# Performance work log

Hardware: AMD Instinct MI355X
Metric: run time of the kernel (lower is better)

## Reference

```python
import jax, jax.numpy as jnp
import numpy as np

N = 50000
E = 800000
EPS = 1e-5


def graph_conv(x, src, dst, ew, W_rel, b_rel, W_root):
    # PyG GraphConv (aggr='add'): lin_rel(sum_j e_ij * x_j) + lin_root(x_i)
    msg = x[src] * ew[:, None]                      # [E, F_in]
    agg = jax.ops.segment_sum(msg, dst, num_segments=N)  # [N, F_in]
    return agg @ W_rel.T + b_rel + x @ W_root.T


def batchnorm_relu(h, gamma, beta):
    mu = jnp.mean(h, axis=0)
    var = jnp.mean(jnp.square(h - mu), axis=0)
    hn = (h - mu) * jax.lax.rsqrt(var + EPS)
    return jax.nn.relu(hn * gamma + beta)


def setup_inputs() -> dict:
    key = jax.random.key(0)
    ks = jax.random.split(key, 16)
    d_in, h, d_out = 128, 256, 64

    def lin(k, fo, fi):
        return jax.random.normal(k, (fo, fi), jnp.float32) * (1.0 / np.sqrt(fi))

    return {
        "x": jax.random.normal(ks[0], (N, d_in), jnp.float32),
        "edge_index": jax.random.randint(ks[1], (2, E), 0, N, jnp.int32),
        "edge_weight": jax.random.uniform(ks[2], (E,), jnp.float32),
        "Wr0": lin(ks[3], h, d_in), "br0": jnp.zeros((h,), jnp.float32), "Wt0": lin(ks[4], h, d_in),
        "g0": jnp.ones((h,), jnp.float32), "be0": jnp.zeros((h,), jnp.float32),
        "Wr1": lin(ks[5], h, h), "br1": jnp.zeros((h,), jnp.float32), "Wt1": lin(ks[6], h, h),
        "g1": jnp.ones((h,), jnp.float32), "be1": jnp.zeros((h,), jnp.float32),
        "Wr2": lin(ks[7], d_out, h), "br2": jnp.zeros((d_out,), jnp.float32), "Wt2": lin(ks[8], d_out, h),
    }


def reference(x, edge_index, edge_weight, Wr0, br0, Wt0, g0, be0,
              Wr1, br1, Wt1, g1, be1, Wr2, br2, Wt2):
    src, dst = edge_index[0], edge_index[1]
    h = graph_conv(x, src, dst, edge_weight, Wr0, br0, Wt0)
    h = batchnorm_relu(h, g0, be0)
    h = graph_conv(h, src, dst, edge_weight, Wr1, br1, Wt1)
    h = batchnorm_relu(h, g1, be1)
    return graph_conv(h, src, dst, edge_weight, Wr2, br2, Wt2)
```

## Files before the change

kernel.cpp:

```cpp
#include <hip/hip_runtime.h>
#include <cstddef>
#include <cstdint>

#define SCAN_B 512

using bf16x8 = __attribute__((ext_vector_type(8))) short;
using f32x4  = __attribute__((ext_vector_type(4))) float;

__device__ __forceinline__ unsigned short f2bf(float f) {
    unsigned int u = __builtin_bit_cast(unsigned int, f);
    return (unsigned short)((u + 0x7FFFu + ((u >> 16) & 1u)) >> 16);
}
__device__ __forceinline__ float bf2f(unsigned short b) {
    unsigned int u = ((unsigned int)b) << 16;
    return __builtin_bit_cast(float, u);
}
__device__ __forceinline__ float i2f(int i) { return __builtin_bit_cast(float, i); }
__device__ __forceinline__ float u2f(unsigned int u) { return __builtin_bit_cast(float, u); }
__device__ __forceinline__ void gload_lds16(const void* g, void* l) {
    __builtin_amdgcn_global_load_lds((const __attribute__((address_space(1))) void*)g,
                                     (__attribute__((address_space(3))) void*)l, 16, 0, 0);
}

__global__ void hist_conv_k(const int* __restrict__ dst, int* __restrict__ counts,
                            int* __restrict__ rank, int E, int histBlocks,
                            const float* __restrict__ x, const float* __restrict__ Wr0,
                            const float* __restrict__ Wt0, const float* __restrict__ Wr1,
                            const float* __restrict__ Wt1, const float* __restrict__ Wr2,
                            const float* __restrict__ Wt2, unsigned short* __restrict__ x_bf,
                            unsigned short* __restrict__ Wr0b, unsigned short* __restrict__ Wt0b,
                            unsigned short* __restrict__ Wr1b, unsigned short* __restrict__ Wt1b,
                            unsigned short* __restrict__ Wr2b, unsigned short* __restrict__ Wt2b,
                            int n4x) {
    if ((int)blockIdx.x < histBlocks) {
        int e = blockIdx.x * 256 + threadIdx.x;
        if (e < E) rank[e] = atomicAdd(&counts[dst[e]], 1);
        return;
    }
    int j = (blockIdx.x - histBlocks) * 256 + threadIdx.x;
    const float* s;
    unsigned short* d;
    if (j < n4x) { s = x; d = x_bf; }
    else {
        j -= n4x;
        if (j < 8192) { s = Wr0; d = Wr0b; }
        else { j -= 8192;
        if (j < 8192) { s = Wt0; d = Wt0b; }
        else { j -= 8192;
        if (j < 16384) { s = Wr1; d = Wr1b; }
        else { j -= 16384;
        if (j < 16384) { s = Wt1; d = Wt1b; }
        else { j -= 16384;
        if (j < 4096) { s = Wr2; d = Wr2b; }
        else { j -= 4096;
        if (j >= 4096) return;
        s = Wt2; d = Wt2b; } } } } }
    }
    float4 v = reinterpret_cast<const float4*>(s)[j];
    ushort4 o;
    o.x = f2bf(v.x); o.y = f2bf(v.y); o.z = f2bf(v.z); o.w = f2bf(v.w);
    reinterpret_cast<ushort4*>(d)[j] = o;
}

__global__ void scan1_k(const int* __restrict__ counts, int* __restrict__ partial,
                        int* __restrict__ blocksum, int Nn) {
    __shared__ int sh[SCAN_B];
    int i = blockIdx.x * SCAN_B + threadIdx.x;
    int v = (i < Nn) ? counts[i] : 0;
    sh[threadIdx.x] = v;
    __syncthreads();
    for (int off = 1; off < SCAN_B; off <<= 1) {
        int t = (threadIdx.x >= (unsigned)off) ? sh[threadIdx.x - off] : 0;
        __syncthreads();
        sh[threadIdx.x] += t;
        __syncthreads();
    }
    if (i < Nn) partial[i] = sh[threadIdx.x];
    if (threadIdx.x == SCAN_B - 1) blocksum[blockIdx.x] = sh[threadIdx.x];
}

__global__ void scan3b_k(const int* __restrict__ partial, const int* __restrict__ blocksum,
                         int* __restrict__ offsets, int Nn) {
    __shared__ int add_s;
    int bx = blockIdx.x;
    if (threadIdx.x < 64) {
        int s = 0;
        for (int j = threadIdx.x; j < bx; j += 64) s += blocksum[j];
        #pragma unroll
        for (int off = 32; off > 0; off >>= 1) s += __shfl_down(s, off, 64);
        if (threadIdx.x == 0) add_s = s;
    }
    __syncthreads();
    int i = bx * SCAN_B + threadIdx.x;
    if (i >= Nn) return;
    offsets[i + 1] = partial[i] + add_s;
    if (i == 0) offsets[0] = 0;
}

__global__ void fill2_k(const int* __restrict__ src, const int* __restrict__ dst,
                        const float* __restrict__ ew, const int* __restrict__ offsets,
                        const int* __restrict__ rank, int2* __restrict__ e_sw, int E) {
    int e = blockIdx.x * blockDim.x + threadIdx.x;
    if (e >= E) return;
    int pos = offsets[dst[e]] + rank[e];
    e_sw[pos] = make_int2(src[e], __builtin_bit_cast(int, ew[e]));
}

__global__ void gather128_k(const unsigned short* __restrict__ x, const int* __restrict__ offsets,
                            const int2* __restrict__ e_sw, unsigned short* __restrict__ agg, int Nn) {
    int wid = __builtin_amdgcn_readfirstlane((blockIdx.x * blockDim.x + threadIdx.x) >> 6);
    int lane = threadIdx.x & 63;
    if (wid >= Nn) return;
    int p = offsets[wid], end = offsets[wid + 1];
    const char* xb = (const char*)x;
    const unsigned loff = lane * 4u;
    float a0 = 0.f, a1 = 0.f;
    for (; p + 8 <= end; p += 8) {
        int2 ee[8];
        #pragma unroll
        for (int i = 0; i < 8; ++i) ee[i] = e_sw[p + i];
        unsigned vv[8];
        #pragma unroll
        for (int i = 0; i < 8; ++i)
            vv[i] = *reinterpret_cast<const unsigned*>(xb + ((unsigned)ee[i].x * 256u + loff));
        #pragma unroll
        for (int i = 0; i < 8; ++i) {
            float w = i2f(ee[i].y);
            a0 += w * u2f(vv[i] << 16); a1 += w * u2f(vv[i] & 0xFFFF0000u);
        }
    }
    for (; p < end; ++p) {
        int2 e0 = e_sw[p];
        unsigned v0 = *reinterpret_cast<const unsigned*>(xb + ((unsigned)e0.x * 256u + loff));
        float w = i2f(e0.y);
        a0 += w * u2f(v0 << 16); a1 += w * u2f(v0 & 0xFFFF0000u);
    }
    unsigned o = (unsigned)f2bf(a0) | ((unsigned)f2bf(a1) << 16);
    *reinterpret_cast<unsigned*>(agg + (size_t)wid * 128 + lane * 2) = o;
}

__global__ void gather_bn_k(const unsigned short* __restrict__ h_raw,
                            const float* __restrict__ sums, const float* __restrict__ sumsq,
                            const float* __restrict__ g, const float* __restrict__ be,
                            const int* __restrict__ offsets, const int2* __restrict__ e_sw,
                            unsigned short* __restrict__ agg, unsigned short* __restrict__ hN,
                            float invN, int Nn, int gBlocks) {
    const int lane = threadIdx.x & 63;
    if ((int)blockIdx.x >= gBlocks) {
        int total4 = Nn * 64;
        int stride = (gridDim.x - gBlocks) * 256;
        for (int t = (blockIdx.x - gBlocks) * 256 + threadIdx.x; t < total4; t += stride) {
            int f0 = (t & 63) * 4;
            float4 sm = *reinterpret_cast<const float4*>(sums + f0);
            float4 sq = *reinterpret_cast<const float4*>(sumsq + f0);
            float4 gg = *reinterpret_cast<const float4*>(g + f0);
            float4 bb = *reinterpret_cast<const float4*>(be + f0);
            float smv[4] = {sm.x, sm.y, sm.z, sm.w};
            float sqv[4] = {sq.x, sq.y, sq.z, sq.w};
            float ggv[4] = {gg.x, gg.y, gg.z, gg.w};
            float bbv[4] = {bb.x, bb.y, bb.z, bb.w};
            ushort4 v = reinterpret_cast<const ushort4*>(h_raw)[t];
            unsigned short vv[4] = {v.x, v.y, v.z, v.w};
            ushort4 o;
            unsigned short* op = &o.x;
            #pragma unroll
            for (int c = 0; c < 4; ++c) {
                float mu = smv[c] * invN;
                float var = sqv[c] * invN - mu * mu;
                float sc = ggv[c] * rsqrtf(var + 1e-5f);
                float sh = bbv[c] - mu * sc;
                op[c] = f2bf(fmaxf(bf2f(vv[c]) * sc + sh, 0.f));
            }
            reinterpret_cast<ushort4*>(hN)[t] = o;
        }
        return;
    }
    int wid = __builtin_amdgcn_readfirstlane((blockIdx.x * blockDim.x + threadIdx.x) >> 6);
    if (wid >= Nn) return;
    int f0 = lane * 4;
    float4 sm = *reinterpret_cast<const float4*>(sums + f0);
    float4 sq = *reinterpret_cast<const float4*>(sumsq + f0);
    float4 gg = *reinterpret_cast<const float4*>(g + f0);
    float4 bb = *reinterpret_cast<const float4*>(be + f0);
    float sc0, sc1, sc2, sc3, sh0, sh1, sh2, sh3;
    {
        float mu, var;
        mu = sm.x * invN; var = sq.x * invN - mu * mu; sc0 = gg.x * rsqrtf(var + 1e-5f); sh0 = bb.x - mu * sc0;
        mu = sm.y * invN; var = sq.y * invN - mu * mu; sc1 = gg.y * rsqrtf(var + 1e-5f); sh1 = bb.y - mu * sc1;
        mu = sm.z * invN; var = sq.z * invN - mu * mu; sc2 = gg.z * rsqrtf(var + 1e-5f); sh2 = bb.z - mu * sc2;
        mu = sm.w * invN; var = sq.w * invN - mu * mu; sc3 = gg.w * rsqrtf(var + 1e-5f); sh3 = bb.w - mu * sc3;
    }
    int p = offsets[wid], end = offsets[wid + 1];
    const char* xb = (const char*)h_raw;
    const unsigned loff = lane * 8u;
    float a0 = 0.f, a1 = 0.f, a2 = 0.f, a3 = 0.f;
    for (; p + 8 <= end; p += 8) {
        int2 ee[8];
        #pragma unroll
        for (int i = 0; i < 8; ++i) ee[i] = e_sw[p + i];
        uint2 vv[8];
        #pragma unroll
        for (int i = 0; i < 8; ++i)
            vv[i] = *reinterpret_cast<const uint2*>(xb + ((unsigned)ee[i].x * 512u + loff));
        #pragma unroll
        for (int i = 0; i < 8; ++i) {
            float w = i2f(ee[i].y);
            a0 += w * fmaxf(u2f(vv[i].x << 16) * sc0 + sh0, 0.f);
            a1 += w * fmaxf(u2f(vv[i].x & 0xFFFF0000u) * sc1 + sh1, 0.f);
            a2 += w * fmaxf(u2f(vv[i].y << 16) * sc2 + sh2, 0.f);
            a3 += w * fmaxf(u2f(vv[i].y & 0xFFFF0000u) * sc3 + sh3, 0.f);
        }
    }
    for (; p < end; ++p) {
        int2 e0 = e_sw[p];
        uint2 v0 = *reinterpret_cast<const uint2*>(xb + ((unsigned)e0.x * 512u + loff));
        float w = i2f(e0.y);
        a0 += w * fmaxf(u2f(v0.x << 16) * sc0 + sh0, 0.f);
        a1 += w * fmaxf(u2f(v0.x & 0xFFFF0000u) * sc1 + sh1, 0.f);
        a2 += w * fmaxf(u2f(v0.y << 16) * sc2 + sh2, 0.f);
        a3 += w * fmaxf(u2f(v0.y & 0xFFFF0000u) * sc3 + sh3, 0.f);
    }
    uint2 o;
    o.x = (unsigned)f2bf(a0) | ((unsigned)f2bf(a1) << 16);
    o.y = (unsigned)f2bf(a2) | ((unsigned)f2bf(a3) << 16);
    *reinterpret_cast<uint2*>(agg + (size_t)wid * 256 + lane * 4) = o;
}

__global__ void gather_out_k(const unsigned short* __restrict__ t, const float* __restrict__ root,
                             const int* __restrict__ offsets, const int2* __restrict__ e_sw,
                             float* __restrict__ out, int Nn) {
    int gt = blockIdx.x * blockDim.x + threadIdx.x;
    int node = gt >> 4;
    int li = gt & 15;
    if (node >= Nn) return;
    int p = offsets[node], end = offsets[node + 1];
    const char* tb = (const char*)t;
    const unsigned loff = li * 8u;
    float a0 = 0.f, a1 = 0.f, a2 = 0.f, a3 = 0.f;
    for (; p + 8 <= end; p += 8) {
        int2 ee[8];
        #pragma unroll
        for (int i = 0; i < 8; ++i) ee[i] = e_sw[p + i];
        uint2 vv[8];
        #pragma unroll
        for (int i = 0; i < 8; ++i)
            vv[i] = *reinterpret_cast<const uint2*>(tb + ((unsigned)ee[i].x * 128u + loff));
        #pragma unroll
        for (int i = 0; i < 8; ++i) {
            float w = i2f(ee[i].y);
            a0 += w * u2f(vv[i].x << 16); a1 += w * u2f(vv[i].x & 0xFFFF0000u);
            a2 += w * u2f(vv[i].y << 16); a3 += w * u2f(vv[i].y & 0xFFFF0000u);
        }
    }
    for (; p < end; ++p) {
        int2 e0 = e_sw[p];
        uint2 v0 = *reinterpret_cast<const uint2*>(tb + ((unsigned)e0.x * 128u + loff));
        float w = i2f(e0.y);
        a0 += w * u2f(v0.x << 16); a1 += w * u2f(v0.x & 0xFFFF0000u);
        a2 += w * u2f(v0.y << 16); a3 += w * u2f(v0.y & 0xFFFF0000u);
    }
    float4 r = *reinterpret_cast<const float4*>(root + (size_t)node * 64 + li * 4);
    float4 o = make_float4(r.x + a0, r.y + a1, r.z + a2, r.w + a3);
    *reinterpret_cast<float4*>(out + (size_t)node * 64 + li * 4) = o;
}

template<int K, int O, int MODE>
__global__ __launch_bounds__(512, 4) void gemm_mfma_k(
        const unsigned short* __restrict__ A, const unsigned short* __restrict__ Wa,
        const unsigned short* __restrict__ X, const unsigned short* __restrict__ Wb,
        const float* __restrict__ bias, unsigned short* __restrict__ out_bf,
        float* __restrict__ out_f, float* __restrict__ sums, float* __restrict__ sumsq,
        int Nn) {
    constexpr int BM = 128, BN = 128;
    constexpr int MI = 4;
    constexpr int OJ = 2;
    constexpr int KSTEPS = K / 32;
    constexpr int NT = (MODE == 0 ? 2 : 1) * KSTEPS;
    __shared__ unsigned short As[2][BM * 32];
    __shared__ unsigned short Bs[2][BN * 32];
    const int tid = threadIdx.x;
    const int w = tid >> 6, l = tid & 63;
    const int wr = w >> 2, wc = w & 3;
    const int lrow = l & 15, kgrp = l >> 4;
    int bx = blockIdx.x;
    bx = (bx & 7) * (gridDim.x >> 3) + (bx >> 3);
    const int m0 = bx * BM;
    const int n0 = blockIdx.y * BN;
    const int srow = tid >> 2, sslot = tid & 3;
    const int gslot = sslot ^ ((srow >> 1) & 3);

    auto stage = [&](int buf, int t) {
        int ph = t / KSTEPS;
        int k0 = (t % KSTEPS) * 32;
        const unsigned short* Ap = (MODE == 0 && ph) ? X : A;
        const unsigned short* Wp = (MODE == 0 && ph) ? Wb : Wa;
        gload_lds16(Ap + (size_t)(m0 + srow) * K + k0 + (gslot << 3), &As[buf][w * 512]);
        gload_lds16(Wp + (size_t)(n0 + srow) * K + k0 + (gslot << 3), &Bs[buf][w * 512]);
    };

    f32x4 acc[MI][OJ];
    #pragma unroll
    for (int i = 0; i < MI; ++i)
        #pragma unroll
        for (int j = 0; j < OJ; ++j) {
            f32x4 z = {0.f, 0.f, 0.f, 0.f};
            acc[i][j] = z;
        }

    stage(0, 0);
    #pragma unroll
    for (int t = 0; t < NT; ++t) {
        const int cur = t & 1;
        asm volatile("s_waitcnt vmcnt(0)" ::: "memory");
        __builtin_amdgcn_sched_barrier(0);
        __builtin_amdgcn_s_barrier();
        __builtin_amdgcn_sched_barrier(0);
        if (t + 1 < NT) stage(cur ^ 1, t + 1);
        bf16x8 a[MI], b[OJ];
        #pragma unroll
        for (int mi = 0; mi < MI; ++mi) {
            int row = wr * 64 + mi * 16 + lrow;
            int slot = kgrp ^ ((row >> 1) & 3);
            a[mi] = *reinterpret_cast<const bf16x8*>(&As[cur][row * 32 + slot * 8]);
        }
        #pragma unroll
        for (int oj = 0; oj < OJ; ++oj) {
            int row = wc * 32 + oj * 16 + lrow;
            int slot = kgrp ^ ((row >> 1) & 3);
            b[oj] = *reinterpret_cast<const bf16x8*>(&Bs[cur][row * 32 + slot * 8]);
        }
        #pragma unroll
        for (int mi = 0; mi < MI; ++mi)
            #pragma unroll
            for (int oj = 0; oj < OJ; ++oj)
                acc[mi][oj] = __builtin_amdgcn_mfma_f32_16x16x32_bf16(
                    a[mi], b[oj], acc[mi][oj], 0, 0, 0);
    }

    if constexpr (MODE == 0) {
        #pragma unroll
        for (int oj = 0; oj < OJ; ++oj) {
            int col = n0 + wc * 32 + oj * 16 + lrow;
            float bcol = bias[col];
            float s = 0.f, q = 0.f;
            #pragma unroll
            for (int mi = 0; mi < MI; ++mi) {
                #pragma unroll
                for (int r = 0; r < 4; ++r) {
                    int row = m0 + wr * 64 + mi * 16 + kgrp * 4 + r;
                    float v = acc[mi][oj][r] + bcol;
                    if (row < Nn) {
                        out_bf[(size_t)row * O + col] = f2bf(v);
                        s += v; q += v * v;
                    }
                }
            }
            s += __shfl_xor(s, 16, 64); q += __shfl_xor(q, 16, 64);
            s += __shfl_xor(s, 32, 64); q += __shfl_xor(q, 32, 64);
            if (kgrp == 0) {
                atomicAdd(&sums[col], s);
                atomicAdd(&sumsq[col], q);
            }
        }
    } else {
        #pragma unroll
        for (int oj = 0; oj < OJ; ++oj) {
            int col = n0 + wc * 32 + oj * 16 + lrow;
            #pragma unroll
            for (int mi = 0; mi < MI; ++mi) {
                #pragma unroll
                for (int r = 0; r < 4; ++r) {
                    int row = m0 + wr * 64 + mi * 16 + kgrp * 4 + r;
                    if (row < Nn) {
                        if (col < 64)
                            out_bf[(size_t)row * 64 + col] = f2bf(acc[mi][oj][r]);
                        else
                            out_f[(size_t)row * 64 + (col - 64)] = acc[mi][oj][r] + bias[col - 64];
                    }
                }
            }
        }
    }
}

__global__ void bn_relu_bf_k(const unsigned short* __restrict__ h, const float* __restrict__ sums,
                             const float* __restrict__ sumsq, const float* __restrict__ g,
                             const float* __restrict__ be, unsigned short* __restrict__ hb,
                             float invN, int total4) {
    int t = blockIdx.x * blockDim.x + threadIdx.x;
    if (t >= total4) return;
    int f0 = (t & 63) * 4;
    float4 sm = *reinterpret_cast<const float4*>(sums + f0);
    float4 sq = *reinterpret_cast<const float4*>(sumsq + f0);
    float4 gg = *reinterpret_cast<const float4*>(g + f0);
    float4 bb = *reinterpret_cast<const float4*>(be + f0);
    float smv[4] = {sm.x, sm.y, sm.z, sm.w};
    float sqv[4] = {sq.x, sq.y, sq.z, sq.w};
    float ggv[4] = {gg.x, gg.y, gg.z, gg.w};
    float bbv[4] = {bb.x, bb.y, bb.z, bb.w};
    ushort4 v = reinterpret_cast<const ushort4*>(h)[t];
    unsigned short vv[4] = {v.x, v.y, v.z, v.w};
    ushort4 o;
    unsigned short* op = &o.x;
    #pragma unroll
    for (int c = 0; c < 4; ++c) {
        float mu = smv[c] * invN;
        float var = sqv[c] * invN - mu * mu;
        float sc = ggv[c] * rsqrtf(var + 1e-5f);
        float sh = bbv[c] - mu * sc;
        op[c] = f2bf(fmaxf(bf2f(vv[c]) * sc + sh, 0.f));
    }
    reinterpret_cast<ushort4*>(hb)[t] = o;
}

extern "C" void kernel_launch(void* const* d_in, const int* in_sizes, int n_in,
                              void* d_out, int out_size, void* d_ws, size_t ws_size,
                              hipStream_t stream) {
    const float* x   = (const float*)d_in[0];
    const int*   ei  = (const int*)d_in[1];
    const float* ew  = (const float*)d_in[2];
    const float* Wr0 = (const float*)d_in[3];
    const float* br0 = (const float*)d_in[4];
    const float* Wt0 = (const float*)d_in[5];
    const float* g0  = (const float*)d_in[6];
    const float* be0 = (const float*)d_in[7];
    const float* Wr1 = (const float*)d_in[8];
    const float* br1 = (const float*)d_in[9];
    const float* Wt1 = (const float*)d_in[10];
    const float* g1  = (const float*)d_in[11];
    const float* be1 = (const float*)d_in[12];
    const float* Wr2 = (const float*)d_in[13];
    const float* br2 = (const float*)d_in[14];
    const float* Wt2 = (const float*)d_in[15];

    const int E  = in_sizes[2];
    const int Nn = in_sizes[0] / 128;
    const size_t NP = 50176;
    const int* src = ei;
    const int* dst = ei + E;

    unsigned short* x_bf   = (unsigned short*)d_ws;
    unsigned short* agg_bf = x_bf + NP * 128;
    unsigned short* h0N    = agg_bf + NP * 256;
    unsigned short* h1N    = h0N + NP * 256;
    unsigned short* h_bf   = h1N + NP * 256;
    unsigned short* t_bf   = h_bf + NP * 256;
    unsigned short* wbf    = t_bf + NP * 64;
    unsigned short* Wr0b = wbf;
    unsigned short* Wt0b = wbf + 32768;
    unsigned short* Wr1b = wbf + 65536;
    unsigned short* Wt1b = wbf + 131072;
    unsigned short* W2cat = wbf + 196608;
    float* root  = (float*)(wbf + 229376);
    int2*  e_sw  = (int2*)(root + NP * 64);
    float* stats = (float*)(e_sw + E);
    int*   counts  = (int*)(stats + 4096);
    int*   partial = counts + Nn;
    int*   blocksum = partial + Nn;
    int*   rank    = blocksum + 512;
    int*   offsets = rank + E;

    dim3 blk(256);
    const int nbScan = (Nn + SCAN_B - 1) / SCAN_B;
    const float invN = 1.0f / (float)Nn;
    const int n4x = Nn * 32;
    const int histBlocks = (E + 255) / 256;
    const int convBlocks = (n4x + 57344 + 255) / 256;

    hipMemsetAsync(stats, 0, (4096 + (size_t)Nn) * sizeof(float), stream);

    hist_conv_k<<<dim3(histBlocks + convBlocks), blk, 0, stream>>>(
        dst, counts, rank, E, histBlocks,
        x, Wr0, Wt0, Wr1, Wt1, Wr2, Wt2,
        x_bf, Wr0b, Wt0b, Wr1b, Wt1b, W2cat, W2cat + 16384, n4x);
    scan1_k<<<dim3(nbScan), dim3(SCAN_B), 0, stream>>>(counts, partial, blocksum, Nn);
    scan3b_k<<<dim3(nbScan), dim3(SCAN_B), 0, stream>>>(partial, blocksum, offsets, Nn);
    fill2_k<<<dim3(histBlocks), blk, 0, stream>>>(src, dst, ew, offsets, rank, e_sw, E);

    const int gatherBlocks = (Nn * 64 + 255) / 256;

    gather128_k<<<dim3(gatherBlocks), blk, 0, stream>>>(x_bf, offsets, e_sw, agg_bf, Nn);
    gemm_mfma_k<128, 256, 0><<<dim3(NP / 128, 2), dim3(512), 0, stream>>>(
        agg_bf, Wr0b, x_bf, Wt0b, br0, h_bf, nullptr, stats + 0, stats + 256, Nn);

    gather_bn_k<<<dim3(gatherBlocks + 2048), blk, 0, stream>>>(
        h_bf, stats + 0, stats + 256, g0, be0, offsets, e_sw,
        agg_bf, h0N, invN, Nn, gatherBlocks);

    gemm_mfma_k<256, 256, 0><<<dim3(NP / 128, 2), dim3(512), 0, stream>>>(
        agg_bf, Wr1b, h0N, Wt1b, br1, h_bf, nullptr, stats + 1024, stats + 1280, Nn);
    bn_relu_bf_k<<<dim3((Nn * 64 + 255) / 256), blk, 0, stream>>>(
        h_bf, stats + 1024, stats + 1280, g1, be1, h1N, invN, Nn * 64);

    gemm_mfma_k<256, 128, 1><<<dim3(NP / 128, 1), dim3(512), 0, stream>>>(
        h1N, W2cat, nullptr, nullptr, br2, t_bf, root, nullptr, nullptr, Nn);
    gather_out_k<<<dim3((Nn * 16 + 255) / 256), blk, 0, stream>>>(
        t_bf, root, offsets, e_sw, (float*)d_out, Nn);
}
```

Before: 296.3 us.

## Merge scan kernels and deepen GEMM K-tile to 64

```diff
diff --git a/kernel.cpp b/kernel.cpp
--- a/kernel.cpp
+++ b/kernel.cpp
@@ -62,38 +62,32 @@
     reinterpret_cast<ushort4*>(d)[j] = o;
 }
 
-__global__ void scan1_k(const int* __restrict__ counts, int* __restrict__ partial,
-                        int* __restrict__ blocksum, int Nn) {
+__global__ void scan_k(const int* __restrict__ counts, int* __restrict__ offsets, int Nn) {
     __shared__ int sh[SCAN_B];
-    int i = blockIdx.x * SCAN_B + threadIdx.x;
+    __shared__ int pre_s;
+    const int bx = blockIdx.x;
+    const int base = bx * SCAN_B;
+    int s = 0;
+    for (int j = threadIdx.x; j < base; j += SCAN_B) s += counts[j];
+    sh[threadIdx.x] = s;
+    __syncthreads();
+    for (int off = SCAN_B / 2; off > 0; off >>= 1) {
+        if ((int)threadIdx.x < off) sh[threadIdx.x] += sh[threadIdx.x + off];
+        __syncthreads();
+    }
+    if (threadIdx.x == 0) pre_s = sh[0];
+    __syncthreads();
+    int i = base + threadIdx.x;
     int v = (i < Nn) ? counts[i] : 0;
     sh[threadIdx.x] = v;
     __syncthreads();
     for (int off = 1; off < SCAN_B; off <<= 1) {
-        int t = (threadIdx.x >= (unsigned)off) ? sh[threadIdx.x - off] : 0;
+        int t = ((int)threadIdx.x >= off) ? sh[threadIdx.x - off] : 0;
         __syncthreads();
         sh[threadIdx.x] += t;
         __syncthreads();
     }
-    if (i < Nn) partial[i] = sh[threadIdx.x];
-    if (threadIdx.x == SCAN_B - 1) blocksum[blockIdx.x] = sh[threadIdx.x];
-}
-
-__global__ void scan3b_k(const int* __restrict__ partial, const int* __restrict__ blocksum,
-                         int* __restrict__ offsets, int Nn) {
-    __shared__ int add_s;
-    int bx = blockIdx.x;
-    if (threadIdx.x < 64) {
-        int s = 0;
-        for (int j = threadIdx.x; j < bx; j += 64) s += blocksum[j];
-        #pragma unroll
-        for (int off = 32; off > 0; off >>= 1) s += __shfl_down(s, off, 64);
-        if (threadIdx.x == 0) add_s = s;
-    }
-    __syncthreads();
-    int i = bx * SCAN_B + threadIdx.x;
-    if (i >= Nn) return;
-    offsets[i + 1] = partial[i] + add_s;
+    if (i < Nn) offsets[i + 1] = sh[threadIdx.x] + pre_s;
     if (i == 0) offsets[0] = 0;
 }
 
@@ -265,7 +259,7 @@
 }
 
 template<int K, int O, int MODE>
-__global__ __launch_bounds__(512, 4) void gemm_mfma_k(
+__global__ __launch_bounds__(512, 2) void gemm_mfma_k(
         const unsigned short* __restrict__ A, const unsigned short* __restrict__ Wa,
         const unsigned short* __restrict__ X, const unsigned short* __restrict__ Wb,
         const float* __restrict__ bias, unsigned short* __restrict__ out_bf,
@@ -274,10 +268,10 @@
     constexpr int BM = 128, BN = 128;
     constexpr int MI = 4;
     constexpr int OJ = 2;
-    constexpr int KSTEPS = K / 32;
-    constexpr int NT = (MODE == 0 ? 2 : 1) * KSTEPS;
-    __shared__ unsigned short As[2][BM * 32];
-    __shared__ unsigned short Bs[2][BN * 32];
+    constexpr int KS64 = K / 64;
+    constexpr int NT = (MODE == 0 ? 2 : 1) * KS64;
+    __shared__ unsigned short As[2][BM * 64];
+    __shared__ unsigned short Bs[2][BN * 64];
     const int tid = threadIdx.x;
     const int w = tid >> 6, l = tid & 63;
     const int wr = w >> 2, wc = w & 3;
@@ -286,16 +280,21 @@
     bx = (bx & 7) * (gridDim.x >> 3) + (bx >> 3);
     const int m0 = bx * BM;
     const int n0 = blockIdx.y * BN;
-    const int srow = tid >> 2, sslot = tid & 3;
-    const int gslot = sslot ^ ((srow >> 1) & 3);
 
     auto stage = [&](int buf, int t) {
-        int ph = t / KSTEPS;
-        int k0 = (t % KSTEPS) * 32;
+        int ph = t / KS64;
+        int k0 = (t % KS64) * 64;
         const unsigned short* Ap = (MODE == 0 && ph) ? X : A;
         const unsigned short* Wp = (MODE == 0 && ph) ? Wb : Wa;
-        gload_lds16(Ap + (size_t)(m0 + srow) * K + k0 + (gslot << 3), &As[buf][w * 512]);
-        gload_lds16(Wp + (size_t)(n0 + srow) * K + k0 + (gslot << 3), &Bs[buf][w * 512]);
+        #pragma unroll
+        for (int i = 0; i < 2; ++i) {
+            int c = i * 512 + tid;
+            int row = c >> 3, slot = c & 7;
+            gload_lds16(Ap + (size_t)(m0 + row) * K + k0 + ((slot ^ (row & 7)) << 3),
+                        &As[buf][(i * 512 + w * 64) * 8]);
+            gload_lds16(Wp + (size_t)(n0 + row) * K + k0 + ((slot ^ (row & 7)) << 3),
+                        &Bs[buf][(i * 512 + w * 64) * 8]);
+        }
     };
 
     f32x4 acc[MI][OJ];
@@ -316,25 +315,28 @@
         __builtin_amdgcn_s_barrier();
         __builtin_amdgcn_sched_barrier(0);
         if (t + 1 < NT) stage(cur ^ 1, t + 1);
-        bf16x8 a[MI], b[OJ];
-        #pragma unroll
-        for (int mi = 0; mi < MI; ++mi) {
-            int row = wr * 64 + mi * 16 + lrow;
-            int slot = kgrp ^ ((row >> 1) & 3);
-            a[mi] = *reinterpret_cast<const bf16x8*>(&As[cur][row * 32 + slot * 8]);
-        }
-        #pragma unroll
-        for (int oj = 0; oj < OJ; ++oj) {
-            int row = wc * 32 + oj * 16 + lrow;
-            int slot = kgrp ^ ((row >> 1) & 3);
-            b[oj] = *reinterpret_cast<const bf16x8*>(&Bs[cur][row * 32 + slot * 8]);
-        }
-        #pragma unroll
-        for (int mi = 0; mi < MI; ++mi)
-            #pragma unroll
-            for (int oj = 0; oj < OJ; ++oj)
-                acc[mi][oj] = __builtin_amdgcn_mfma_f32_16x16x32_bf16(
-                    a[mi], b[oj], acc[mi][oj], 0, 0, 0);
+        #pragma unroll
+        for (int ks = 0; ks < 2; ++ks) {
+            bf16x8 a[MI], b[OJ];
+            #pragma unroll
+            for (int mi = 0; mi < MI; ++mi) {
+                int row = wr * 64 + mi * 16 + lrow;
+                int slot = (ks * 4 + kgrp) ^ (row & 7);
+                a[mi] = *reinterpret_cast<const bf16x8*>(&As[cur][row * 64 + slot * 8]);
+            }
+            #pragma unroll
+            for (int oj = 0; oj < OJ; ++oj) {
+                int row = wc * 32 + oj * 16 + lrow;
+                int slot = (ks * 4 + kgrp) ^ (row & 7);
+                b[oj] = *reinterpret_cast<const bf16x8*>(&Bs[cur][row * 64 + slot * 8]);
+            }
+            #pragma unroll
+            for (int mi = 0; mi < MI; ++mi)
+                #pragma unroll
+                for (int oj = 0; oj < OJ; ++oj)
+                    acc[mi][oj] = __builtin_amdgcn_mfma_f32_16x16x32_bf16(
+                        a[mi], b[oj], acc[mi][oj], 0, 0, 0);
+        }
     }
 
     if constexpr (MODE == 0) {
@@ -455,9 +457,7 @@
     int2*  e_sw  = (int2*)(root + NP * 64);
     float* stats = (float*)(e_sw + E);
     int*   counts  = (int*)(stats + 4096);
-    int*   partial = counts + Nn;
-    int*   blocksum = partial + Nn;
-    int*   rank    = blocksum + 512;
+    int*   rank    = counts + Nn;
     int*   offsets = rank + E;
 
     dim3 blk(256);
@@ -473,8 +473,7 @@
         dst, counts, rank, E, histBlocks,
         x, Wr0, Wt0, Wr1, Wt1, Wr2, Wt2,
         x_bf, Wr0b, Wt0b, Wr1b, Wt1b, W2cat, W2cat + 16384, n4x);
-    scan1_k<<<dim3(nbScan), dim3(SCAN_B), 0, stream>>>(counts, partial, blocksum, Nn);
-    scan3b_k<<<dim3(nbScan), dim3(SCAN_B), 0, stream>>>(partial, blocksum, offsets, Nn);
+    scan_k<<<dim3(nbScan), dim3(SCAN_B), 0, stream>>>(counts, offsets, Nn);
     fill2_k<<<dim3(histBlocks), blk, 0, stream>>>(src, dst, ew, offsets, rank, e_sw, E);
 
     const int gatherBlocks = (Nn * 64 + 255) / 256;
```

Measured after the change: 311.5 us. 1.05x slower.
